# Optimization experiments

Hardware: AMD Instinct MI355X
Metric: run time of the kernel (lower is better)

Reference implementation:

```python
import jax, jax.numpy as jnp
import numpy as np

B, T, L, W = 4, 4096, 64, 8          # batch, text len, media tokens, max_window_per_audio
DIM, DIM_A, H, DH = 2048, 1024, 8, 64
INNER = H * DH
LN_EPS = 1e-5


def setup_inputs() -> dict:
    key = jax.random.key(0)
    ks = jax.random.split(key, 8)
    x = jax.random.normal(ks[0], (B, T, DIM), jnp.float32)
    media = jax.random.normal(ks[1], (B, L, 1, DIM_A), jnp.float32)
    media_mask = jax.random.uniform(ks[2], (B, L, 1)) > 0.1
    # sparse media markers (~8 per row); ensure at least one per row
    media_locations = (jax.random.uniform(ks[3], (B, T)) < (8.0 / T)).astype(jnp.int32)
    media_locations = media_locations.at[:, 0].set(1)
    Wq = jax.random.normal(ks[4], (DIM, INNER), jnp.float32) / np.sqrt(DIM).astype(np.float32)
    Wkv = jax.random.normal(ks[5], (DIM_A, 2 * INNER), jnp.float32) / np.sqrt(DIM_A).astype(np.float32)
    Wout = jax.random.normal(ks[6], (INNER, DIM), jnp.float32) / np.sqrt(INNER).astype(np.float32)
    gamma = jnp.ones((DIM,), jnp.float32)
    beta = jnp.zeros((DIM,), jnp.float32)
    return dict(x=x, media=media, media_mask=media_mask, media_locations=media_locations,
                Wq=Wq, Wkv=Wkv, Wout=Wout, gamma=gamma, beta=beta)


def reference(x, media, media_mask, media_locations, Wq, Wkv, Wout, gamma, beta):
    scale = DH ** -0.5
    # LayerNorm (biased variance, like torch)
    mu = x.mean(-1, keepdims=True)
    var = x.var(-1, keepdims=True)
    xn = (x - mu) * jax.lax.rsqrt(var + LN_EPS) * gamma + beta
    # projections
    q = (xn @ Wq).reshape(B, T, H, DH).transpose(0, 2, 1, 3) * scale   # [B,h,T,dh]
    kv = media.reshape(B, L, DIM_A) @ Wkv
    k, v = jnp.split(kv, 2, axis=-1)
    k = k.reshape(B, L, H, DH).transpose(0, 2, 1, 3)                   # [B,h,L,dh]
    v = v.reshape(B, L, H, DH).transpose(0, 2, 1, 3)
    sim = jnp.einsum('bhid,bhjd->bhij', q, k)                          # [B,h,T,L]
    big = jnp.finfo(sim.dtype).max
    # media validity mask
    mm = media_mask.reshape(B, 1, 1, L)
    sim = jnp.where(mm, sim, -big)
    # few-shot window mask (only_attend_immediate_media=False):
    # token t attends windows [0, max(#media at <=t, 1) * W)
    cum = jnp.cumsum((media_locations != 0).astype(jnp.int32), axis=1)  # [B,T]
    end = jnp.maximum(cum, 1) * W                                       # [B,T]
    fsm = jnp.arange(L)[None, None, :] < end[:, :, None]                # [B,T,L]
    sim = jnp.where(fsm[:, None], sim, -big)
    sim = sim - jax.lax.stop_gradient(sim.max(-1, keepdims=True))
    attn = jax.nn.softmax(sim, axis=-1)
    out = jnp.einsum('bhij,bhjd->bhid', attn, v)                        # [B,h,T,dh]
    out = out.transpose(0, 2, 1, 3).reshape(B, T, INNER)
    return out @ Wout
```

## Files before the change

### kernel.cpp

```cpp
#include <hip/hip_runtime.h>
#include <float.h>

typedef __bf16 bf16;
typedef __bf16 bf16x8 __attribute__((ext_vector_type(8)));
typedef float f32x4 __attribute__((ext_vector_type(4)));
typedef float f32x16 __attribute__((ext_vector_type(16)));

#define GAS __attribute__((address_space(1)))
#define LAS __attribute__((address_space(3)))

__device__ __forceinline__ void gload_lds16(const void* g, void* l) {
  __builtin_amdgcn_global_load_lds((const GAS unsigned int*)g, (LAS unsigned int*)l, 16, 0, 0);
}

__global__ __launch_bounds__(512, 2) void qattn(
    const bf16* __restrict__ xn, const bf16* __restrict__ wqT,
    const bf16* __restrict__ kvb, const int* __restrict__ mk,
    const int* __restrict__ endw, bf16* __restrict__ aob) {
  constexpr int K = 2048;
  __shared__ __align__(16) bf16 Abuf[3][256 * 64];
  __shared__ __align__(16) bf16 Bbuf[3][128 * 64];
  const int tid = threadIdx.x, lane = tid & 63;
  const int w = tid >> 6, wr = w >> 1, wc = w & 1;
  const int g = lane >> 4, fr = lane & 15;

  const int gx = gridDim.x;
  const int nwg = gx * gridDim.y;
  int lid = blockIdx.y * gx + blockIdx.x;
  {
    const int qq = nwg >> 3, rr = nwg & 7;
    const int xcd = lid & 7, pos = lid >> 3;
    lid = (xcd < rr ? xcd * (qq + 1) : rr * (qq + 1) + (xcd - rr) * qq) + pos;
  }
  const int bx = lid % gx, by = lid / gx;
  const size_t m0 = (size_t)by * 256;
  const int n0 = bx * 128;

  const int nt = K >> 6;
  const int srow = tid >> 3, sslot = tid & 7;

  f32x4 acc[4][4] = {};

  auto stage = [&](int t) {
    const int s = t % 3;
    const int kt = t << 6;
#pragma unroll
    for (int c = 0; c < 4; ++c) {
      const int r = c * 64 + srow;
      gload_lds16(xn + (m0 + r) * (size_t)K + kt + ((sslot ^ (r & 7)) << 3),
                  &Abuf[s][c * 4096 + w * 512]);
    }
#pragma unroll
    for (int c = 0; c < 2; ++c) {
      const int r = c * 64 + srow;
      gload_lds16(wqT + (size_t)(n0 + r) * K + kt + ((sslot ^ (r & 7)) << 3),
                  &Bbuf[s][c * 4096 + w * 512]);
    }
  };
  auto rdA = [&](int s, int mi, int ks) {
    const int r = wr * 64 + mi * 16 + fr;
    return *(const bf16x8*)&Abuf[s][r * 64 + ((((ks << 2) | g) ^ (r & 7)) << 3)];
  };
  auto rdB = [&](int s, int ni, int ks) {
    const int r = wc * 64 + ni * 16 + fr;
    return *(const bf16x8*)&Bbuf[s][r * 64 + ((((ks << 2) | g) ^ (r & 7)) << 3)];
  };
  auto compute = [&](int t) {
    const int s = t % 3;
    bf16x8 bv[4][2];
#pragma unroll
    for (int ni = 0; ni < 4; ++ni)
#pragma unroll
      for (int ks = 0; ks < 2; ++ks) bv[ni][ks] = rdB(s, ni, ks);
    __builtin_amdgcn_s_setprio(1);
#pragma unroll
    for (int mi = 0; mi < 4; ++mi)
#pragma unroll
      for (int ks = 0; ks < 2; ++ks) {
        const bf16x8 av = rdA(s, mi, ks);
#pragma unroll
        for (int ni = 0; ni < 4; ++ni)
          acc[mi][ni] = __builtin_amdgcn_mfma_f32_16x16x32_bf16(
              av, bv[ni][ks], acc[mi][ni], 0, 0, 0);
      }
    __builtin_amdgcn_s_setprio(0);
  };

  stage(0);
  stage(1);
  for (int t = 0; t < nt - 1; ++t) {
    __builtin_amdgcn_sched_barrier(0);
    asm volatile("s_waitcnt vmcnt(6)" ::: "memory");
    __builtin_amdgcn_s_barrier();
    __builtin_amdgcn_sched_barrier(0);
    if (t + 2 < nt) stage(t + 2);
    compute(t);
  }
  __builtin_amdgcn_sched_barrier(0);
  asm volatile("s_waitcnt vmcnt(0)" ::: "memory");
  __builtin_amdgcn_s_barrier();
  __builtin_amdgcn_sched_barrier(0);
  compute(nt - 1);

  __builtin_amdgcn_s_barrier();
  __builtin_amdgcn_sched_barrier(0);

  const int b = (int)(m0 >> 12);
  bf16* QP = &Abuf[0][0] + w * 4096;
  bf16* Klds = &Bbuf[0][0];
  bf16* Vlds = &Bbuf[1][0];

#pragma unroll
  for (int mi = 0; mi < 4; ++mi)
#pragma unroll
    for (int ni = 0; ni < 4; ++ni)
#pragma unroll
      for (int rg = 0; rg < 4; ++rg) {
        const int row = mi * 16 + g * 4 + rg, col = ni * 16 + fr;
        QP[row * 64 + (((col >> 3) ^ (row & 7)) << 3) + (col & 7)] =
            (bf16)acc[mi][ni][rg];
      }

#pragma unroll
  for (int j = 0; j < 2; ++j) {
    const int idx = j * 512 + tid;
    const int head = idx >> 9, l = (idx >> 3) & 63, sl = idx & 7;
    gload_lds16(kvb + (size_t)(b * 64 + l) * 1024 + (2 * bx + head) * 64 +
                    ((sl ^ (l & 7)) << 3),
                Klds + (j * 512 + w * 64) * 8);
  }
#pragma unroll
  for (int j = 0; j < 2; ++j) {
    const int idx = j * 512 + tid;
    const int head = idx >> 9, l = (idx >> 3) & 63, sg = idx & 7;
    bf16x8 vv = *(const bf16x8*)&kvb[(size_t)(b * 64 + l) * 1024 + 512 +
                                     (2 * bx + head) * 64 + sg * 8];
#pragma unroll
    for (int e = 0; e < 8; ++e) {
      const int dh = sg * 8 + e;
      Vlds[head * 4096 + dh * 64 + (((l >> 3) ^ (dh & 7)) << 3) + (l & 7)] =
          vv[e];
    }
  }
  asm volatile("s_waitcnt vmcnt(0)" ::: "memory");
  __syncthreads();

  f32x4 sacc[4][4] = {};
#pragma unroll
  for (int ks = 0; ks < 2; ++ks) {
    bf16x8 aq[4], bk[4];
#pragma unroll
    for (int mi = 0; mi < 4; ++mi) {
      const int r = mi * 16 + fr;
      aq[mi] = *(const bf16x8*)&QP[r * 64 + ((((ks << 2) | g) ^ (r & 7)) << 3)];
    }
#pragma unroll
    for (int ni = 0; ni < 4; ++ni) {
      const int l = ni * 16 + fr;
      bk[ni] = *(const bf16x8*)&Klds[wc * 4096 + l * 64 +
                                     ((((ks << 2) | g) ^ (l & 7)) << 3)];
    }
#pragma unroll
    for (int mi = 0; mi < 4; ++mi)
#pragma unroll
      for (int ni = 0; ni < 4; ++ni)
        sacc[mi][ni] = __builtin_amdgcn_mfma_f32_16x16x32_bf16(
            aq[mi], bk[ni], sacc[mi][ni], 0, 0, 0);
  }

#pragma unroll
  for (int mi = 0; mi < 4; ++mi) {
    const int4 ev4 = *(const int4*)&endw[m0 + wr * 64 + mi * 16 + g * 4];
    const int ev[4] = {ev4.x, ev4.y, ev4.z, ev4.w};
    float p[4][4];
#pragma unroll
    for (int ni = 0; ni < 4; ++ni) {
      const int l = ni * 16 + fr;
      const bool mv = (mk[b * 64 + l] != 0);
#pragma unroll
      for (int rg = 0; rg < 4; ++rg)
        p[ni][rg] = (mv && (l < ev[rg])) ? sacc[mi][ni][rg] : -FLT_MAX;
    }
#pragma unroll
    for (int rg = 0; rg < 4; ++rg) {
      float m = fmaxf(fmaxf(p[0][rg], p[1][rg]), fmaxf(p[2][rg], p[3][rg]));
      m = fmaxf(m, __shfl_xor(m, 1));
      m = fmaxf(m, __shfl_xor(m, 2));
      m = fmaxf(m, __shfl_xor(m, 4));
      m = fmaxf(m, __shfl_xor(m, 8));
      float sum = 0.f;
#pragma unroll
      for (int ni = 0; ni < 4; ++ni) {
        p[ni][rg] = __expf(p[ni][rg] - m);
        sum += p[ni][rg];
      }
      sum += __shfl_xor(sum, 1);
      sum += __shfl_xor(sum, 2);
      sum += __shfl_xor(sum, 4);
      sum += __shfl_xor(sum, 8);
      const float inv = 1.f / sum;
#pragma unroll
      for (int ni = 0; ni < 4; ++ni) p[ni][rg] *= inv;
    }
#pragma unroll
    for (int ni = 0; ni < 4; ++ni) {
      const int l = ni * 16 + fr;
#pragma unroll
      for (int rg = 0; rg < 4; ++rg) {
        const int row = mi * 16 + g * 4 + rg;
        QP[row * 64 + (((l >> 3) ^ (row & 7)) << 3) + (l & 7)] =
            (bf16)p[ni][rg];
      }
    }
  }

  f32x4 oacc[4][4] = {};
#pragma unroll
  for (int ks = 0; ks < 2; ++ks) {
    bf16x8 pa[4], bv[4];
#pragma unroll
    for (int mi = 0; mi < 4; ++mi) {
      const int r = mi * 16 + fr;
      pa[mi] = *(const bf16x8*)&QP[r * 64 + ((((ks << 2) | g) ^ (r & 7)) << 3)];
    }
#pragma unroll
    for (int nd = 0; nd < 4; ++nd) {
      const int dh = nd * 16 + fr;
      bv[nd] = *(const bf16x8*)&Vlds[wc * 4096 + dh * 64 +
                                     ((((ks << 2) | g) ^ (dh & 7)) << 3)];
    }
#pragma unroll
    for (int mi = 0; mi < 4; ++mi)
#pragma unroll
      for (int nd = 0; nd < 4; ++nd)
        oacc[mi][nd] = __builtin_amdgcn_mfma_f32_16x16x32_bf16(
            pa[mi], bv[nd], oacc[mi][nd], 0, 0, 0);
  }
#pragma unroll
  for (int mi = 0; mi < 4; ++mi)
#pragma unroll
    for (int nd = 0; nd < 4; ++nd)
#pragma unroll
      for (int rg = 0; rg < 4; ++rg) {
        const size_t t = m0 + wr * 64 + mi * 16 + g * 4 + rg;
        aob[t * 512 + (2 * bx + wc) * 64 + nd * 16 + fr] =
            (bf16)oacc[mi][nd][rg];
      }
}

template <int OUT_BF16>
__global__ __launch_bounds__(512, 2) void gemm_big(
    const bf16* __restrict__ A, const bf16* __restrict__ Bt,
    void* __restrict__ Cv, int M, int N, int K) {
  __shared__ __align__(16) bf16 Abuf[3][256 * 64];
  __shared__ __align__(16) bf16 Bbuf[3][128 * 64];
  const int tid = threadIdx.x, lane = tid & 63;
  const int w = tid >> 6, wr = w >> 2, wc = w & 3;
  const int l31 = lane & 31, hi = lane >> 5;

  const int gx = gridDim.x;
  const int nwg = gx * gridDim.y;
  int lid = blockIdx.y * gx + blockIdx.x;
  {
    const int qq = nwg >> 3, rr = nwg & 7;
    const int xcd = lid & 7, pos = lid >> 3;
    lid = (xcd < rr ? xcd * (qq + 1) : rr * (qq + 1) + (xcd - rr) * qq) + pos;
  }
  const int bx = lid % gx, by = lid / gx;
  const size_t m0 = (size_t)by * 256, n0 = (size_t)bx * 128;

  const int nt = K >> 6;
  const int srow = tid >> 3;
  const int sslot = tid & 7;

  f32x16 acc[4] = {};

  auto stage = [&](int t) {
    const int s = t % 3;
    const int kt = t << 6;
#pragma unroll
    for (int c = 0; c < 4; ++c) {
      const int r = c * 64 + srow;
      gload_lds16(A + (m0 + r) * (size_t)K + kt + ((sslot ^ (r & 7)) << 3),
                  &Abuf[s][c * 4096 + w * 512]);
    }
#pragma unroll
    for (int c = 0; c < 2; ++c) {
      const int r = c * 64 + srow;
      gload_lds16(Bt + (n0 + r) * (size_t)K + kt + ((sslot ^ (r & 7)) << 3),
                  &Bbuf[s][c * 4096 + w * 512]);
    }
  };

  auto rdA = [&](int s, int mi, int ks) {
    const int r = wr * 128 + mi * 32 + l31;
    return *(const bf16x8*)&Abuf[s][r * 64 + ((((ks << 1) | hi) ^ (r & 7)) << 3)];
  };
  auto rdB = [&](int s, int ks) {
    const int r = wc * 32 + l31;
    return *(const bf16x8*)&Bbuf[s][r * 64 + ((((ks << 1) | hi) ^ (r & 7)) << 3)];
  };

  auto compute = [&](int t) {
    const int s = t % 3;
    bf16x8 bv[4];
#pragma unroll
    for (int ks = 0; ks < 4; ++ks) bv[ks] = rdB(s, ks);
    __builtin_amdgcn_s_setprio(1);
#pragma unroll
    for (int ks = 0; ks < 4; ++ks)
#pragma unroll
      for (int mi = 0; mi < 4; ++mi) {
        const bf16x8 av = rdA(s, mi, ks);
        acc[mi] = __builtin_amdgcn_mfma_f32_32x32x16_bf16(av, bv[ks], acc[mi],
                                                          0, 0, 0);
      }
    __builtin_amdgcn_s_setprio(0);
  };

  stage(0);
  stage(1);
  for (int t = 0; t < nt - 1; ++t) {
    __builtin_amdgcn_sched_barrier(0);
    asm volatile("s_waitcnt vmcnt(6)" ::: "memory");
    __builtin_amdgcn_s_barrier();
    __builtin_amdgcn_sched_barrier(0);
    if (t + 2 < nt) stage(t + 2);
    compute(t);
  }
  __builtin_amdgcn_sched_barrier(0);
  asm volatile("s_waitcnt vmcnt(0)" ::: "memory");
  __builtin_amdgcn_s_barrier();
  __builtin_amdgcn_sched_barrier(0);
  compute(nt - 1);

#pragma unroll
  for (int mi = 0; mi < 4; ++mi)
#pragma unroll
    for (int rg = 0; rg < 16; ++rg) {
      const size_t row =
          m0 + wr * 128 + mi * 32 + (rg & 3) + ((rg >> 2) << 3) + (hi << 2);
      const size_t col = n0 + wc * 32 + l31;
      if (OUT_BF16)
        ((bf16*)Cv)[row * (size_t)N + col] = (bf16)acc[mi][rg];
      else
        ((float*)Cv)[row * (size_t)N + col] = acc[mi][rg];
    }
}

template <int OUT_BF16>
__global__ __launch_bounds__(256, 2) void gemm_bt(
    const bf16* __restrict__ A, const bf16* __restrict__ Bt,
    void* __restrict__ Cv, int M, int N, int K) {
  __shared__ bf16 As[128 * 32];
  __shared__ bf16 Bs[128 * 32];
  const int tid = threadIdx.x;
  const int lane = tid & 63, w = tid >> 6;
  const int wr = w >> 1, wc = w & 1;

  const int gx = gridDim.x;
  const int nwg = gx * gridDim.y;
  int lid = blockIdx.y * gx + blockIdx.x;
  {
    const int qq = nwg >> 3, rr = nwg & 7;
    const int xcd = lid & 7, pos = lid >> 3;
    lid = (xcd < rr ? xcd * (qq + 1) : rr * (qq + 1) + (xcd - rr) * qq) + pos;
  }
  const int bx = lid % gx, by = lid / gx;
  const size_t m0 = (size_t)by * 128, n0 = (size_t)bx * 128;

  const int srow = lane >> 2, sslot = lane & 3;
  const int g = lane >> 4, fr = lane & 15;

  f32x4 acc[4][4] = {};

  for (int kt = 0; kt < K; kt += 32) {
    __syncthreads();
#pragma unroll
    for (int j = 0; j < 2; ++j) {
      const int c = 2 * w + j;
      const int r = c * 16 + srow;
      const int ks = (sslot ^ (r & 3)) << 3;
      gload_lds16(A + (m0 + r) * K + kt + ks, &As[c * 512]);
      gload_lds16(Bt + (n0 + r) * K + kt + ks, &Bs[c * 512]);
    }
    __syncthreads();
    bf16x8 av[4], bv[4];
#pragma unroll
    for (int mi = 0; mi < 4; ++mi) {
      const int r = wr * 64 + mi * 16 + fr;
      av[mi] = *(const bf16x8*)&As[r * 32 + ((g ^ (r & 3)) << 3)];
    }
#pragma unroll
    for (int ni = 0; ni < 4; ++ni) {
      const int r = wc * 64 + ni * 16 + fr;
      bv[ni] = *(const bf16x8*)&Bs[r * 32 + ((g ^ (r & 3)) << 3)];
    }
#pragma unroll
    for (int mi = 0; mi < 4; ++mi)
#pragma unroll
      for (int ni = 0; ni < 4; ++ni)
        acc[mi][ni] = __builtin_amdgcn_mfma_f32_16x16x32_bf16(
            av[mi], bv[ni], acc[mi][ni], 0, 0, 0);
  }

#pragma unroll
  for (int mi = 0; mi < 4; ++mi)
#pragma unroll
    for (int ni = 0; ni < 4; ++ni)
#pragma unroll
      for (int rg = 0; rg < 4; ++rg) {
        const size_t row = m0 + wr * 64 + mi * 16 + g * 4 + rg;
        const size_t col = n0 + wc * 64 + ni * 16 + fr;
        if (OUT_BF16)
          ((bf16*)Cv)[row * (size_t)N + col] = (bf16)acc[mi][ni][rg];
        else
          ((float*)Cv)[row * (size_t)N + col] = acc[mi][ni][rg];
      }
}

__device__ __forceinline__ void transp64(const float* __restrict__ src,
                                         bf16* __restrict__ dst, int R, int C,
                                         float scale, int tile, float* lds) {
  const int tilesC = C >> 6;
  const int tr = tile / tilesC, tc = tile % tilesC;
  const int r0 = tr << 6, c0 = tc << 6;
  const int tid = threadIdx.x;
  const int lr = tid >> 6, lc = tid & 63;
#pragma unroll
  for (int j = 0; j < 16; ++j) {
    const int r = j * 4 + lr;
    lds[r * 65 + lc] = src[(size_t)(r0 + r) * C + c0 + lc];
  }
  __syncthreads();
#pragma unroll
  for (int j = 0; j < 16; ++j) {
    const int rr = j * 4 + lr;
    dst[(size_t)(c0 + rr) * R + r0 + lc] = (bf16)(lds[lc * 65 + rr] * scale);
  }
}

__global__ __launch_bounds__(256) void prep_all(
    const float* __restrict__ x, const float* __restrict__ gamma,
    const float* __restrict__ beta, bf16* __restrict__ xn,
    const float* __restrict__ Wq, bf16* __restrict__ wqT,
    const float* __restrict__ Wkv, bf16* __restrict__ wkvT,
    const float* __restrict__ Wout, bf16* __restrict__ woT,
    const float* __restrict__ media, bf16* __restrict__ medb,
    const int* __restrict__ mloc, int* __restrict__ endw,
    const unsigned char* __restrict__ mraw, int* __restrict__ mk) {
  __shared__ float shf[64 * 65];
  const int blk = blockIdx.x, tid = threadIdx.x;

  if (blk < 16384) {
    const size_t base = (size_t)blk * 2048 + tid * 8;
    f32x4 v0 = *(const f32x4*)(x + base);
    f32x4 v1 = *(const f32x4*)(x + base + 4);
    float s = 0.f, q2 = 0.f;
#pragma unroll
    for (int j = 0; j < 4; ++j) {
      s += v0[j] + v1[j];
      q2 += v0[j] * v0[j] + v1[j] * v1[j];
    }
    for (int off = 32; off > 0; off >>= 1) {
      s += __shfl_down(s, off);
      q2 += __shfl_down(q2, off);
    }
    const int lane = tid & 63, wv = tid >> 6;
    if (lane == 0) { shf[wv] = s; shf[4 + wv] = q2; }
    __syncthreads();
    s = shf[0] + shf[1] + shf[2] + shf[3];
    q2 = shf[4] + shf[5] + shf[6] + shf[7];
    const float mu = s * (1.f / 2048.f);
    const float var = q2 * (1.f / 2048.f) - mu * mu;
    const float rs = rsqrtf(var + 1e-5f);
    f32x4 g0 = *(const f32x4*)(gamma + tid * 8);
    f32x4 g1 = *(const f32x4*)(gamma + tid * 8 + 4);
    f32x4 b0 = *(const f32x4*)(beta + tid * 8);
    f32x4 b1 = *(const f32x4*)(beta + tid * 8 + 4);
    bf16x8 o;
#pragma unroll
    for (int j = 0; j < 4; ++j) {
      o[j] = (bf16)((v0[j] - mu) * rs * g0[j] + b0[j]);
      o[4 + j] = (bf16)((v1[j] - mu) * rs * g1[j] + b1[j]);
    }
    *(bf16x8*)(xn + base) = o;
  } else if (blk < 16640) {
    transp64(Wq, wqT, 2048, 512, 0.125f, blk - 16384, shf);
  } else if (blk < 16896) {
    transp64(Wkv, wkvT, 1024, 1024, 1.f, blk - 16640, shf);
  } else if (blk < 17152) {
    transp64(Wout, woT, 512, 2048, 1.f, blk - 16896, shf);
  } else if (blk < 18176) {
    const int i = (blk - 17152) * 256 + tid;
    medb[i] = (bf16)media[i];
  } else if (blk < 18180) {
    int* part = (int*)shf;
    const int b = blk - 18176;
    int loc[16];
    int s = 0;
    const int base = b * 4096 + tid * 16;
#pragma unroll
    for (int j = 0; j < 16; ++j) {
      loc[j] = (mloc[base + j] != 0) ? 1 : 0;
      s += loc[j];
    }
    part[tid] = s;
    __syncthreads();
    for (int off = 1; off < 256; off <<= 1) {
      int v = (tid >= off) ? part[tid - off] : 0;
      __syncthreads();
      part[tid] += v;
      __syncthreads();
    }
    int c = (tid > 0) ? part[tid - 1] : 0;
#pragma unroll
    for (int j = 0; j < 16; ++j) {
      c += loc[j];
      int e = (c > 1 ? c : 1) << 3;
      endw[base + j] = e > 64 ? 64 : e;
    }
  } else {
    int* isbool = (int*)shf;
    if (tid == 0) *isbool = 0;
    __syncthreads();
    const unsigned char v = mraw[tid];
    if ((tid & 3) != 0 && v != 0) atomicOr(isbool, 1);
    __syncthreads();
    mk[tid] = (*isbool) ? (int)mraw[tid] : ((const int*)mraw)[tid];
  }
}

extern "C" void kernel_launch(void* const* d_in, const int* in_sizes, int n_in,
                              void* d_out, int out_size, void* d_ws,
                              size_t ws_size, hipStream_t stream) {
  const float* x = (const float*)d_in[0];
  const float* media = (const float*)d_in[1];
  const unsigned char* mraw = (const unsigned char*)d_in[2];
  const int* mloc = (const int*)d_in[3];
  const float* Wq = (const float*)d_in[4];
  const float* Wkv = (const float*)d_in[5];
  const float* Wout = (const float*)d_in[6];
  const float* gamma = (const float*)d_in[7];
  const float* beta = (const float*)d_in[8];
  float* out = (float*)d_out;

  bf16* xn = (bf16*)d_out;

  char* ws = (char*)d_ws;
  size_t off = 0;
  auto carve = [&](size_t bytes) {
    void* p = ws + off;
    off += (bytes + 255) & ~(size_t)255;
    return p;
  };
  bf16* aob = (bf16*)carve((size_t)16384 * 512 * 2);
  bf16* kvb = (bf16*)carve((size_t)256 * 1024 * 2);
  bf16* wqT = (bf16*)carve((size_t)512 * 2048 * 2);
  bf16* wkvT = (bf16*)carve((size_t)1024 * 1024 * 2);
  bf16* woT = (bf16*)carve((size_t)2048 * 512 * 2);
  bf16* medb = (bf16*)carve((size_t)256 * 1024 * 2);
  int* endw = (int*)carve((size_t)4 * 4096 * 4);
  int* mk = (int*)carve(256 * 4);
  (void)ws_size;
  (void)in_sizes;
  (void)n_in;
  (void)out_size;

  prep_all<<<18181, 256, 0, stream>>>(x, gamma, beta, xn, Wq, wqT, Wkv, wkvT,
                                      Wout, woT, media, medb, mloc, endw, mraw,
                                      mk);

  gemm_bt<1><<<dim3(8, 2), 256, 0, stream>>>(medb, wkvT, kvb, 256, 1024, 1024);

  qattn<<<dim3(4, 64), 512, 0, stream>>>(xn, wqT, kvb, mk, endw, aob);

  gemm_big<0><<<dim3(16, 64), 512, 0, stream>>>(aob, woT, out, 16384, 2048,
                                                512);
}
```

Baseline: 177.7 us.

## Merge all stages into one persistent cooperative kernel with grid syncs

Replaces the four separate launches (prep, KV GEMM, fused Q-attention, output GEMM) with a single cooperative kernel of 256 workgroups. Grid-wide syncs separate the phases: preprocessing, the KV projection on 16 blocks, and then the attention and output GEMM, with each block computing four 256x128 output tiles in a loop. The aim is to remove launch overhead and inter-kernel gaps. In exchange, the layernorm phase now uses only 256 blocks, most blocks sit idle during the KV GEMM, and the output GEMM runs with fixed persistent tiling, which may lower occupancy and overlap.

```diff
diff --git a/kernel.cpp b/kernel.cpp
--- a/kernel.cpp
+++ b/kernel.cpp
@@ -1,7 +1,11 @@
 #include <hip/hip_runtime.h>
+#include <hip/hip_cooperative_groups.h>
 #include <float.h>
 
+namespace cg = cooperative_groups;
+
 typedef __bf16 bf16;
+typedef __bf16 bf16x4v __attribute__((ext_vector_type(4)));
 typedef __bf16 bf16x8 __attribute__((ext_vector_type(8)));
 typedef float f32x4 __attribute__((ext_vector_type(4)));
 typedef float f32x16 __attribute__((ext_vector_type(16)));
@@ -13,546 +17,524 @@
   __builtin_amdgcn_global_load_lds((const GAS unsigned int*)g, (LAS unsigned int*)l, 16, 0, 0);
 }
 
-__global__ __launch_bounds__(512, 2) void qattn(
-    const bf16* __restrict__ xn, const bf16* __restrict__ wqT,
-    const bf16* __restrict__ kvb, const int* __restrict__ mk,
-    const int* __restrict__ endw, bf16* __restrict__ aob) {
-  constexpr int K = 2048;
-  __shared__ __align__(16) bf16 Abuf[3][256 * 64];
-  __shared__ __align__(16) bf16 Bbuf[3][128 * 64];
-  const int tid = threadIdx.x, lane = tid & 63;
-  const int w = tid >> 6, wr = w >> 1, wc = w & 1;
-  const int g = lane >> 4, fr = lane & 15;
-
-  const int gx = gridDim.x;
-  const int nwg = gx * gridDim.y;
-  int lid = blockIdx.y * gx + blockIdx.x;
+struct MP {
+  const float* x;
+  const float* media;
+  const unsigned char* mraw;
+  const int* mloc;
+  const float* Wq;
+  const float* Wkv;
+  const float* Wout;
+  const float* gamma;
+  const float* beta;
+  float* out;
+  bf16* xn;
+  bf16* aob;
+  bf16* kvb;
+  bf16* wqT;
+  bf16* wkvT;
+  bf16* woT;
+  bf16* medb;
+  int* endw;
+  int* mk;
+};
+
+__global__ __launch_bounds__(512, 2) void mega(MP p) {
+  __shared__ __align__(16) char smem[147456];
+  const int tid = threadIdx.x, lane = tid & 63, w = tid >> 6;
+  const int lid = blockIdx.x;
+  const int lidx = ((lid & 7) << 5) | (lid >> 3);
+
+  if (lid < 4) {
+    int* part = (int*)smem;
+    const int b = lid;
+    int loc[8];
+    int s = 0;
+    const int base = b * 4096 + tid * 8;
+#pragma unroll
+    for (int j = 0; j < 8; ++j) {
+      loc[j] = (p.mloc[base + j] != 0) ? 1 : 0;
+      s += loc[j];
+    }
+    part[tid] = s;
+    __syncthreads();
+    for (int off = 1; off < 512; off <<= 1) {
+      int v = (tid >= off) ? part[tid - off] : 0;
+      __syncthreads();
+      part[tid] += v;
+      __syncthreads();
+    }
+    int c = (tid > 0) ? part[tid - 1] : 0;
+#pragma unroll
+    for (int j = 0; j < 8; ++j) {
+      c += loc[j];
+      int e = (c > 1 ? c : 1) << 3;
+      p.endw[base + j] = e > 64 ? 64 : e;
+    }
+  } else if (lid == 4) {
+    int* isbool = (int*)smem;
+    if (tid == 0) *isbool = 0;
+    __syncthreads();
+    if (tid < 256) {
+      const unsigned char v = p.mraw[tid];
+      if ((tid & 3) != 0 && v != 0) atomicOr(isbool, 1);
+    }
+    __syncthreads();
+    if (tid < 256)
+      p.mk[tid] = (*isbool) ? (int)p.mraw[tid] : ((const int*)p.mraw)[tid];
+  }
+  __syncthreads();
+
   {
-    const int qq = nwg >> 3, rr = nwg & 7;
-    const int xcd = lid & 7, pos = lid >> 3;
-    lid = (xcd < rr ? xcd * (qq + 1) : rr * (qq + 1) + (xcd - rr) * qq) + pos;
-  }
-  const int bx = lid % gx, by = lid / gx;
-  const size_t m0 = (size_t)by * 256;
-  const int n0 = bx * 128;
-
-  const int nt = K >> 6;
-  const int srow = tid >> 3, sslot = tid & 7;
-
-  f32x4 acc[4][4] = {};
-
-  auto stage = [&](int t) {
-    const int s = t % 3;
-    const int kt = t << 6;
-#pragma unroll
-    for (int c = 0; c < 4; ++c) {
-      const int r = c * 64 + srow;
-      gload_lds16(xn + (m0 + r) * (size_t)K + kt + ((sslot ^ (r & 7)) << 3),
-                  &Abuf[s][c * 4096 + w * 512]);
-    }
-#pragma unroll
-    for (int c = 0; c < 2; ++c) {
-      const int r = c * 64 + srow;
-      gload_lds16(wqT + (size_t)(n0 + r) * K + kt + ((sslot ^ (r & 7)) << 3),
-                  &Bbuf[s][c * 4096 + w * 512]);
-    }
-  };
-  auto rdA = [&](int s, int mi, int ks) {
-    const int r = wr * 64 + mi * 16 + fr;
-    return *(const bf16x8*)&Abuf[s][r * 64 + ((((ks << 2) | g) ^ (r & 7)) << 3)];
-  };
-  auto rdB = [&](int s, int ni, int ks) {
-    const int r = wc * 64 + ni * 16 + fr;
-    return *(const bf16x8*)&Bbuf[s][r * 64 + ((((ks << 2) | g) ^ (r & 7)) << 3)];
-  };
-  auto compute = [&](int t) {
-    const int s = t % 3;
-    bf16x8 bv[4][2];
-#pragma unroll
-    for (int ni = 0; ni < 4; ++ni)
-#pragma unroll
-      for (int ks = 0; ks < 2; ++ks) bv[ni][ks] = rdB(s, ni, ks);
-    __builtin_amdgcn_s_setprio(1);
+    const int i0 = lid * 1024 + tid;
+    p.medb[i0] = (bf16)p.media[i0];
+    p.medb[i0 + 512] = (bf16)p.media[i0 + 512];
+  }
+
+  {
+    float* lds = (float*)smem;
+#pragma unroll 1
+    for (int j3 = 0; j3 < 3; ++j3) {
+      const int job = lid + j3 * 256;
+      const float* src;
+      bf16* dst;
+      int R, C, t0;
+      float sc;
+      if (job < 256) {
+        src = p.Wq; dst = p.wqT; R = 2048; C = 512; sc = 0.125f; t0 = job;
+      } else if (job < 512) {
+        src = p.Wkv; dst = p.wkvT; R = 1024; C = 1024; sc = 1.f; t0 = job - 256;
+      } else {
+        src = p.Wout; dst = p.woT; R = 512; C = 2048; sc = 1.f; t0 = job - 512;
+      }
+      const int tilesC = C >> 6;
+      const int r0 = (t0 / tilesC) << 6, c0 = (t0 % tilesC) << 6;
+      const int lr = tid >> 6, lc = tid & 63;
+#pragma unroll
+      for (int j = 0; j < 8; ++j) {
+        const int r = j * 8 + lr;
+        lds[r * 65 + lc] = src[(size_t)(r0 + r) * C + c0 + lc];
+      }
+      __syncthreads();
+#pragma unroll
+      for (int j = 0; j < 8; ++j) {
+        const int rr = j * 8 + lr;
+        dst[(size_t)(c0 + rr) * R + r0 + lc] = (bf16)(lds[lc * 65 + rr] * sc);
+      }
+      __syncthreads();
+    }
+  }
+
+  {
+#pragma unroll 1
+    for (int i = 0; i < 8; ++i) {
+      const int row = (lid << 6) + (i << 3) + w;
+      const float* xr = p.x + (size_t)row * 2048;
+      float s = 0.f, q2 = 0.f;
+#pragma unroll
+      for (int j = 0; j < 8; ++j) {
+        f32x4 v = *(const f32x4*)(xr + j * 256 + lane * 4);
+        s += v[0] + v[1] + v[2] + v[3];
+        q2 += v[0] * v[0] + v[1] * v[1] + v[2] * v[2] + v[3] * v[3];
+      }
+#pragma unroll
+      for (int off = 32; off > 0; off >>= 1) {
+        s += __shfl_down(s, off);
+        q2 += __shfl_down(q2, off);
+      }
+      s = __shfl(s, 0);
+      q2 = __shfl(q2, 0);
+      const float mu = s * (1.f / 2048.f);
+      const float rs = rsqrtf(q2 * (1.f / 2048.f) - mu * mu + 1e-5f);
+#pragma unroll
+      for (int j = 0; j < 8; ++j) {
+        f32x4 v = *(const f32x4*)(xr + j * 256 + lane * 4);
+        f32x4 gg = *(const f32x4*)(p.gamma + j * 256 + lane * 4);
+        f32x4 bb = *(const f32x4*)(p.beta + j * 256 + lane * 4);
+        bf16x4v o;
+#pragma unroll
+        for (int e = 0; e < 4; ++e) o[e] = (bf16)((v[e] - mu) * rs * gg[e] + bb[e]);
+        *(bf16x4v*)(p.xn + (size_t)row * 2048 + j * 256 + lane * 4) = o;
+      }
+    }
+  }
+
+  cg::this_grid().sync();
+
+  if (lid < 16) {
+    bf16* As = (bf16*)smem;
+    bf16* Bs = (bf16*)(smem + 8192);
+    const int m0k = (lid >> 3) * 128, n0k = (lid & 7) * 128;
+    const int wr = w >> 2, wc = w & 3;
+    const int g = lane >> 4, fr = lane & 15;
+    const int srow = tid >> 2, sslot = tid & 3;
+    f32x4 acc[4][2] = {};
+    for (int kt = 0; kt < 1024; kt += 32) {
+      __syncthreads();
+      gload_lds16(
+          p.medb + (size_t)(m0k + srow) * 1024 + kt + ((sslot ^ (srow & 3)) << 3),
+          As + w * 512);
+      gload_lds16(
+          p.wkvT + (size_t)(n0k + srow) * 1024 + kt + ((sslot ^ (srow & 3)) << 3),
+          Bs + w * 512);
+      __syncthreads();
+      bf16x8 av[4], bv[2];
+#pragma unroll
+      for (int mi = 0; mi < 4; ++mi) {
+        const int r = wr * 64 + mi * 16 + fr;
+        av[mi] = *(const bf16x8*)&As[r * 32 + ((g ^ (r & 3)) << 3)];
+      }
+#pragma unroll
+      for (int ni = 0; ni < 2; ++ni) {
+        const int r = wc * 32 + ni * 16 + fr;
+        bv[ni] = *(const bf16x8*)&Bs[r * 32 + ((g ^ (r & 3)) << 3)];
+      }
+#pragma unroll
+      for (int mi = 0; mi < 4; ++mi)
+#pragma unroll
+        for (int ni = 0; ni < 2; ++ni)
+          acc[mi][ni] = __builtin_amdgcn_mfma_f32_16x16x32_bf16(
+              av[mi], bv[ni], acc[mi][ni], 0, 0, 0);
+    }
 #pragma unroll
     for (int mi = 0; mi < 4; ++mi)
 #pragma unroll
-      for (int ks = 0; ks < 2; ++ks) {
-        const bf16x8 av = rdA(s, mi, ks);
-#pragma unroll
-        for (int ni = 0; ni < 4; ++ni)
-          acc[mi][ni] = __builtin_amdgcn_mfma_f32_16x16x32_bf16(
-              av, bv[ni][ks], acc[mi][ni], 0, 0, 0);
-      }
-    __builtin_amdgcn_s_setprio(0);
-  };
-
-  stage(0);
-  stage(1);
-  for (int t = 0; t < nt - 1; ++t) {
+      for (int ni = 0; ni < 2; ++ni)
+#pragma unroll
+        for (int rg = 0; rg < 4; ++rg) {
+          const int row = m0k + wr * 64 + mi * 16 + g * 4 + rg;
+          const int col = n0k + wc * 32 + ni * 16 + fr;
+          p.kvb[(size_t)row * 1024 + col] = (bf16)acc[mi][ni][rg];
+        }
+  }
+
+  cg::this_grid().sync();
+
+  {
+    bf16* AB = (bf16*)smem;
+    bf16* BB = (bf16*)(smem + 98304);
+    auto Ab = [&](int s) { return AB + s * (256 * 64); };
+    auto Bb = [&](int s) { return BB + s * (128 * 64); };
+    constexpr int K = 2048;
+    const int wr = w >> 1, wc = w & 1;
+    const int g = lane >> 4, fr = lane & 15;
+    const int bx = lidx & 3, by = lidx >> 2;
+    const size_t m0 = (size_t)by * 256;
+    const int n0 = bx * 128;
+    const int nt = K >> 6;
+    const int srow = tid >> 3, sslot = tid & 7;
+
+    f32x4 acc[4][4] = {};
+
+    auto stage = [&](int t) {
+      const int s = t % 3;
+      const int kt = t << 6;
+#pragma unroll
+      for (int c = 0; c < 4; ++c) {
+        const int r = c * 64 + srow;
+        gload_lds16(p.xn + (m0 + r) * (size_t)K + kt + ((sslot ^ (r & 7)) << 3),
+                    Ab(s) + c * 4096 + w * 512);
+      }
+#pragma unroll
+      for (int c = 0; c < 2; ++c) {
+        const int r = c * 64 + srow;
+        gload_lds16(
+            p.wqT + (size_t)(n0 + r) * K + kt + ((sslot ^ (r & 7)) << 3),
+            Bb(s) + c * 4096 + w * 512);
+      }
+    };
+    auto rdA = [&](int s, int mi, int ks) {
+      const int r = wr * 64 + mi * 16 + fr;
+      return *(const bf16x8*)(Ab(s) + r * 64 + ((((ks << 2) | g) ^ (r & 7)) << 3));
+    };
+    auto rdB = [&](int s, int ni, int ks) {
+      const int r = wc * 64 + ni * 16 + fr;
+      return *(const bf16x8*)(Bb(s) + r * 64 + ((((ks << 2) | g) ^ (r & 7)) << 3));
+    };
+    auto compute = [&](int t) {
+      const int s = t % 3;
+      bf16x8 bv[4][2];
+#pragma unroll
+      for (int ni = 0; ni < 4; ++ni)
+#pragma unroll
+        for (int ks = 0; ks < 2; ++ks) bv[ni][ks] = rdB(s, ni, ks);
+      __builtin_amdgcn_s_setprio(1);
+#pragma unroll
+      for (int mi = 0; mi < 4; ++mi)
+#pragma unroll
+        for (int ks = 0; ks < 2; ++ks) {
+          const bf16x8 av = rdA(s, mi, ks);
+#pragma unroll
+          for (int ni = 0; ni < 4; ++ni)
+            acc[mi][ni] = __builtin_amdgcn_mfma_f32_16x16x32_bf16(
+                av, bv[ni][ks], acc[mi][ni], 0, 0, 0);
+        }
+      __builtin_amdgcn_s_setprio(0);
+    };
+
+    stage(0);
+    stage(1);
+    for (int t = 0; t < nt - 1; ++t) {
+      __builtin_amdgcn_sched_barrier(0);
+      asm volatile("s_waitcnt vmcnt(6)" ::: "memory");
+      __builtin_amdgcn_s_barrier();
+      __builtin_amdgcn_sched_barrier(0);
+      if (t + 2 < nt) stage(t + 2);
+      compute(t);
+    }
     __builtin_amdgcn_sched_barrier(0);
-    asm volatile("s_waitcnt vmcnt(6)" ::: "memory");
+    asm volatile("s_waitcnt vmcnt(0)" ::: "memory");
     __builtin_amdgcn_s_barrier();
     __builtin_amdgcn_sched_barrier(0);
-    if (t + 2 < nt) stage(t + 2);
-    compute(t);
-  }
-  __builtin_amdgcn_sched_barrier(0);
-  asm volatile("s_waitcnt vmcnt(0)" ::: "memory");
-  __builtin_amdgcn_s_barrier();
-  __builtin_amdgcn_sched_barrier(0);
-  compute(nt - 1);
-
-  __builtin_amdgcn_s_barrier();
-  __builtin_amdgcn_sched_barrier(0);
-
-  const int b = (int)(m0 >> 12);
-  bf16* QP = &Abuf[0][0] + w * 4096;
-  bf16* Klds = &Bbuf[0][0];
-  bf16* Vlds = &Bbuf[1][0];
-
-#pragma unroll
-  for (int mi = 0; mi < 4; ++mi)
-#pragma unroll
-    for (int ni = 0; ni < 4; ++ni)
-#pragma unroll
-      for (int rg = 0; rg < 4; ++rg) {
-        const int row = mi * 16 + g * 4 + rg, col = ni * 16 + fr;
-        QP[row * 64 + (((col >> 3) ^ (row & 7)) << 3) + (col & 7)] =
-            (bf16)acc[mi][ni][rg];
-      }
-
-#pragma unroll
-  for (int j = 0; j < 2; ++j) {
-    const int idx = j * 512 + tid;
-    const int head = idx >> 9, l = (idx >> 3) & 63, sl = idx & 7;
-    gload_lds16(kvb + (size_t)(b * 64 + l) * 1024 + (2 * bx + head) * 64 +
-                    ((sl ^ (l & 7)) << 3),
-                Klds + (j * 512 + w * 64) * 8);
-  }
-#pragma unroll
-  for (int j = 0; j < 2; ++j) {
-    const int idx = j * 512 + tid;
-    const int head = idx >> 9, l = (idx >> 3) & 63, sg = idx & 7;
-    bf16x8 vv = *(const bf16x8*)&kvb[(size_t)(b * 64 + l) * 1024 + 512 +
-                                     (2 * bx + head) * 64 + sg * 8];
-#pragma unroll
-    for (int e = 0; e < 8; ++e) {
-      const int dh = sg * 8 + e;
-      Vlds[head * 4096 + dh * 64 + (((l >> 3) ^ (dh & 7)) << 3) + (l & 7)] =
-          vv[e];
-    }
-  }
-  asm volatile("s_waitcnt vmcnt(0)" ::: "memory");
-  __syncthreads();
-
-  f32x4 sacc[4][4] = {};
-#pragma unroll
-  for (int ks = 0; ks < 2; ++ks) {
-    bf16x8 aq[4], bk[4];
-#pragma unroll
-    for (int mi = 0; mi < 4; ++mi) {
-      const int r = mi * 16 + fr;
-      aq[mi] = *(const bf16x8*)&QP[r * 64 + ((((ks << 2) | g) ^ (r & 7)) << 3)];
-    }
-#pragma unroll
-    for (int ni = 0; ni < 4; ++ni) {
-      const int l = ni * 16 + fr;
-      bk[ni] = *(const bf16x8*)&Klds[wc * 4096 + l * 64 +
-                                     ((((ks << 2) | g) ^ (l & 7)) << 3)];
-    }
-#pragma unroll
-    for (int mi = 0; mi < 4; ++mi)
-#pragma unroll
-      for (int ni = 0; ni < 4; ++ni)
-        sacc[mi][ni] = __builtin_amdgcn_mfma_f32_16x16x32_bf16(
-            aq[mi], bk[ni], sacc[mi][ni], 0, 0, 0);
-  }
-
-#pragma unroll
-  for (int mi = 0; mi < 4; ++mi) {
-    const int4 ev4 = *(const int4*)&endw[m0 + wr * 64 + mi * 16 + g * 4];
-    const int ev[4] = {ev4.x, ev4.y, ev4.z, ev4.w};
-    float p[4][4];
-#pragma unroll
-    for (int ni = 0; ni < 4; ++ni) {
-      const int l = ni * 16 + fr;
-      const bool mv = (mk[b * 64 + l] != 0);
-#pragma unroll
-      for (int rg = 0; rg < 4; ++rg)
-        p[ni][rg] = (mv && (l < ev[rg])) ? sacc[mi][ni][rg] : -FLT_MAX;
-    }
-#pragma unroll
-    for (int rg = 0; rg < 4; ++rg) {
-      float m = fmaxf(fmaxf(p[0][rg], p[1][rg]), fmaxf(p[2][rg], p[3][rg]));
-      m = fmaxf(m, __shfl_xor(m, 1));
-      m = fmaxf(m, __shfl_xor(m, 2));
-      m = fmaxf(m, __shfl_xor(m, 4));
-      m = fmaxf(m, __shfl_xor(m, 8));
-      float sum = 0.f;
-#pragma unroll
-      for (int ni = 0; ni < 4; ++ni) {
-        p[ni][rg] = __expf(p[ni][rg] - m);
-        sum += p[ni][rg];
-      }
-      sum += __shfl_xor(sum, 1);
-      sum += __shfl_xor(sum, 2);
-      sum += __shfl_xor(sum, 4);
-      sum += __shfl_xor(sum, 8);
-      const float inv = 1.f / sum;
-#pragma unroll
-      for (int ni = 0; ni < 4; ++ni) p[ni][rg] *= inv;
-    }
-#pragma unroll
-    for (int ni = 0; ni < 4; ++ni) {
-      const int l = ni * 16 + fr;
-#pragma unroll
-      for (int rg = 0; rg < 4; ++rg) {
-        const int row = mi * 16 + g * 4 + rg;
-        QP[row * 64 + (((l >> 3) ^ (row & 7)) << 3) + (l & 7)] =
-            (bf16)p[ni][rg];
-      }
-    }
-  }
-
-  f32x4 oacc[4][4] = {};
-#pragma unroll
-  for (int ks = 0; ks < 2; ++ks) {
-    bf16x8 pa[4], bv[4];
-#pragma unroll
-    for (int mi = 0; mi < 4; ++mi) {
-      const int r = mi * 16 + fr;
-      pa[mi] = *(const bf16x8*)&QP[r * 64 + ((((ks << 2) | g) ^ (r & 7)) << 3)];
-    }
-#pragma unroll
-    for (int nd = 0; nd < 4; ++nd) {
-      const int dh = nd * 16 + fr;
-      bv[nd] = *(const bf16x8*)&Vlds[wc * 4096 + dh * 64 +
-                                     ((((ks << 2) | g) ^ (dh & 7)) << 3)];
-    }
-#pragma unroll
-    for (int mi = 0; mi < 4; ++mi)
-#pragma unroll
-      for (int nd = 0; nd < 4; ++nd)
-        oacc[mi][nd] = __builtin_amdgcn_mfma_f32_16x16x32_bf16(
-            pa[mi], bv[nd], oacc[mi][nd], 0, 0, 0);
-  }
-#pragma unroll
-  for (int mi = 0; mi < 4; ++mi)
-#pragma unroll
-    for (int nd = 0; nd < 4; ++nd)
-#pragma unroll
-      for (int rg = 0; rg < 4; ++rg) {
-        const size_t t = m0 + wr * 64 + mi * 16 + g * 4 + rg;
-        aob[t * 512 + (2 * bx + wc) * 64 + nd * 16 + fr] =
-            (bf16)oacc[mi][nd][rg];
-      }
-}
-
-template <int OUT_BF16>
-__global__ __launch_bounds__(512, 2) void gemm_big(
-    const bf16* __restrict__ A, const bf16* __restrict__ Bt,
-    void* __restrict__ Cv, int M, int N, int K) {
-  __shared__ __align__(16) bf16 Abuf[3][256 * 64];
-  __shared__ __align__(16) bf16 Bbuf[3][128 * 64];
-  const int tid = threadIdx.x, lane = tid & 63;
-  const int w = tid >> 6, wr = w >> 2, wc = w & 3;
-  const int l31 = lane & 31, hi = lane >> 5;
-
-  const int gx = gridDim.x;
-  const int nwg = gx * gridDim.y;
-  int lid = blockIdx.y * gx + blockIdx.x;
-  {
-    const int qq = nwg >> 3, rr = nwg & 7;
-    const int xcd = lid & 7, pos = lid >> 3;
-    lid = (xcd < rr ? xcd * (qq + 1) : rr * (qq + 1) + (xcd - rr) * qq) + pos;
-  }
-  const int bx = lid % gx, by = lid / gx;
-  const size_t m0 = (size_t)by * 256, n0 = (size_t)bx * 128;
-
-  const int nt = K >> 6;
-  const int srow = tid >> 3;
-  const int sslot = tid & 7;
-
-  f32x16 acc[4] = {};
-
-  auto stage = [&](int t) {
-    const int s = t % 3;
-    const int kt = t << 6;
-#pragma unroll
-    for (int c = 0; c < 4; ++c) {
-      const int r = c * 64 + srow;
-      gload_lds16(A + (m0 + r) * (size_t)K + kt + ((sslot ^ (r & 7)) << 3),
-                  &Abuf[s][c * 4096 + w * 512]);
-    }
-#pragma unroll
-    for (int c = 0; c < 2; ++c) {
-      const int r = c * 64 + srow;
-      gload_lds16(Bt + (n0 + r) * (size_t)K + kt + ((sslot ^ (r & 7)) << 3),
-                  &Bbuf[s][c * 4096 + w * 512]);
-    }
-  };
-
-  auto rdA = [&](int s, int mi, int ks) {
-    const int r = wr * 128 + mi * 32 + l31;
-    return *(const bf16x8*)&Abuf[s][r * 64 + ((((ks << 1) | hi) ^ (r & 7)) << 3)];
-  };
-  auto rdB = [&](int s, int ks) {
-    const int r = wc * 32 + l31;
-    return *(const bf16x8*)&Bbuf[s][r * 64 + ((((ks << 1) | hi) ^ (r & 7)) << 3)];
-  };
-
-  auto compute = [&](int t) {
-    const int s = t % 3;
-    bf16x8 bv[4];
-#pragma unroll
-    for (int ks = 0; ks < 4; ++ks) bv[ks] = rdB(s, ks);
-    __builtin_amdgcn_s_setprio(1);
-#pragma unroll
-    for (int ks = 0; ks < 4; ++ks)
-#pragma unroll
-      for (int mi = 0; mi < 4; ++mi) {
-        const bf16x8 av = rdA(s, mi, ks);
-        acc[mi] = __builtin_amdgcn_mfma_f32_32x32x16_bf16(av, bv[ks], acc[mi],
-                                                          0, 0, 0);
-      }
-    __builtin_amdgcn_s_setprio(0);
-  };
-
-  stage(0);
-  stage(1);
-  for (int t = 0; t < nt - 1; ++t) {
-    __builtin_amdgcn_sched_barrier(0);
-    asm volatile("s_waitcnt vmcnt(6)" ::: "memory");
+    compute(nt - 1);
+
     __builtin_amdgcn_s_barrier();
     __builtin_amdgcn_sched_barrier(0);
-    if (t + 2 < nt) stage(t + 2);
-    compute(t);
-  }
-  __builtin_amdgcn_sched_barrier(0);
-  asm volatile("s_waitcnt vmcnt(0)" ::: "memory");
-  __builtin_amdgcn_s_barrier();
-  __builtin_amdgcn_sched_barrier(0);
-  compute(nt - 1);
-
-#pragma unroll
-  for (int mi = 0; mi < 4; ++mi)
-#pragma unroll
-    for (int rg = 0; rg < 16; ++rg) {
-      const size_t row =
-          m0 + wr * 128 + mi * 32 + (rg & 3) + ((rg >> 2) << 3) + (hi << 2);
-      const size_t col = n0 + wc * 32 + l31;
-      if (OUT_BF16)
-        ((bf16*)Cv)[row * (size_t)N + col] = (bf16)acc[mi][rg];
-      else
-        ((float*)Cv)[row * (size_t)N + col] = acc[mi][rg];
-    }
-}
-
-template <int OUT_BF16>
-__global__ __launch_bounds__(256, 2) void gemm_bt(
-    const bf16* __restrict__ A, const bf16* __restrict__ Bt,
-    void* __restrict__ Cv, int M, int N, int K) {
-  __shared__ bf16 As[128 * 32];
-  __shared__ bf16 Bs[128 * 32];
-  const int tid = threadIdx.x;
-  const int lane = tid & 63, w = tid >> 6;
-  const int wr = w >> 1, wc = w & 1;
-
-  const int gx = gridDim.x;
-  const int nwg = gx * gridDim.y;
-  int lid = blockIdx.y * gx + blockIdx.x;
+
+    const int b = (int)(m0 >> 12);
+    bf16* QP = Ab(0) + w * 4096;
+    bf16* Klds = Bb(0);
+    bf16* Vlds = Bb(1);
+
+#pragma unroll
+    for (int mi = 0; mi < 4; ++mi)
+#pragma unroll
+      for (int ni = 0; ni < 4; ++ni)
+#pragma unroll
+        for (int rg = 0; rg < 4; ++rg) {
+          const int row = mi * 16 + g * 4 + rg, col = ni * 16 + fr;
+          QP[row * 64 + (((col >> 3) ^ (row & 7)) << 3) + (col & 7)] =
+              (bf16)acc[mi][ni][rg];
+        }
+
+#pragma unroll
+    for (int j = 0; j < 2; ++j) {
+      const int idx = j * 512 + tid;
+      const int head = idx >> 9, l = (idx >> 3) & 63, sl = idx & 7;
+      gload_lds16(p.kvb + (size_t)(b * 64 + l) * 1024 + (2 * bx + head) * 64 +
+                      ((sl ^ (l & 7)) << 3),
+                  Klds + (j * 512 + w * 64) * 8);
+    }
+#pragma unroll
+    for (int j = 0; j < 2; ++j) {
+      const int idx = j * 512 + tid;
+      const int head = idx >> 9, l = (idx >> 3) & 63, sg = idx & 7;
+      bf16x8 vv = *(const bf16x8*)&p.kvb[(size_t)(b * 64 + l) * 1024 + 512 +
+                                         (2 * bx + head) * 64 + sg * 8];
+#pragma unroll
+      for (int e = 0; e < 8; ++e) {
+        const int dh = sg * 8 + e;
+        Vlds[head * 4096 + dh * 64 + (((l >> 3) ^ (dh & 7)) << 3) + (l & 7)] =
+            vv[e];
+      }
+    }
+    asm volatile("s_waitcnt vmcnt(0)" ::: "memory");
+    __syncthreads();
+
+    f32x4 sacc[4][4] = {};
+#pragma unroll
+    for (int ks = 0; ks < 2; ++ks) {
+      bf16x8 aq[4], bk[4];
+#pragma unroll
+      for (int mi = 0; mi < 4; ++mi) {
+        const int r = mi * 16 + fr;
+        aq[mi] = *(const bf16x8*)&QP[r * 64 + ((((ks << 2) | g) ^ (r & 7)) << 3)];
+      }
+#pragma unroll
+      for (int ni = 0; ni < 4; ++ni) {
+        const int l = ni * 16 + fr;
+        bk[ni] = *(const bf16x8*)&Klds[wc * 4096 + l * 64 +
+                                       ((((ks << 2) | g) ^ (l & 7)) << 3)];
+      }
+#pragma unroll
+      for (int mi = 0; mi < 4; ++mi)
+#pragma unroll
+        for (int ni = 0; ni < 4; ++ni)
+          sacc[mi][ni] = __builtin_amdgcn_mfma_f32_16x16x32_bf16(
+              aq[mi], bk[ni], sacc[mi][ni], 0, 0, 0);
+    }
+
+#pragma unroll
+    for (int mi = 0; mi < 4; ++mi) {
+      const int4 ev4 = *(const int4*)&p.endw[m0 + wr * 64 + mi * 16 + g * 4];
+      const int ev[4] = {ev4.x, ev4.y, ev4.z, ev4.w};
+      float pp[4][4];
+#pragma unroll
+      for (int ni = 0; ni < 4; ++ni) {
+        const int l = ni * 16 + fr;
+        const bool mv = (p.mk[b * 64 + l] != 0);
+#pragma unroll
+        for (int rg = 0; rg < 4; ++rg)
+          pp[ni][rg] = (mv && (l < ev[rg])) ? sacc[mi][ni][rg] : -FLT_MAX;
+      }
+#pragma unroll
+      for (int rg = 0; rg < 4; ++rg) {
+        float m = fmaxf(fmaxf(pp[0][rg], pp[1][rg]), fmaxf(pp[2][rg], pp[3][rg]));
+        m = fmaxf(m, __shfl_xor(m, 1));
+        m = fmaxf(m, __shfl_xor(m, 2));
+        m = fmaxf(m, __shfl_xor(m, 4));
+        m = fmaxf(m, __shfl_xor(m, 8));
+        float sum = 0.f;
+#pragma unroll
+        for (int ni = 0; ni < 4; ++ni) {
+          pp[ni][rg] = __expf(pp[ni][rg] - m);
+          sum += pp[ni][rg];
+        }
+        sum += __shfl_xor(sum, 1);
+        sum += __shfl_xor(sum, 2);
+        sum += __shfl_xor(sum, 4);
+        sum += __shfl_xor(sum, 8);
+        const float inv = 1.f / sum;
+#pragma unroll
+        for (int ni = 0; ni < 4; ++ni) pp[ni][rg] *= inv;
+      }
+#pragma unroll
+      for (int ni = 0; ni < 4; ++ni) {
+        const int l = ni * 16 + fr;
+#pragma unroll
+        for (int rg = 0; rg < 4; ++rg) {
+          const int row = mi * 16 + g * 4 + rg;
+          QP[row * 64 + (((l >> 3) ^ (row & 7)) << 3) + (l & 7)] =
+              (bf16)pp[ni][rg];
+        }
+      }
+    }
+
+    f32x4 oacc[4][4] = {};
+#pragma unroll
+    for (int ks = 0; ks < 2; ++ks) {
+      bf16x8 pa[4], bv[4];
+#pragma unroll
+      for (int mi = 0; mi < 4; ++mi) {
+        const int r = mi * 16 + fr;
+        pa[mi] = *(const bf16x8*)&QP[r * 64 + ((((ks << 2) | g) ^ (r & 7)) << 3)];
+      }
+#pragma unroll
+      for (int nd = 0; nd < 4; ++nd) {
+        const int dh = nd * 16 + fr;
+        bv[nd] = *(const bf16x8*)&Vlds[wc * 4096 + dh * 64 +
+                                       ((((ks << 2) | g) ^ (dh & 7)) << 3)];
+      }
+#pragma unroll
+      for (int mi = 0; mi < 4; ++mi)
+#pragma unroll
+        for (int nd = 0; nd < 4; ++nd)
+          oacc[mi][nd] = __builtin_amdgcn_mfma_f32_16x16x32_bf16(
+              pa[mi], bv[nd], oacc[mi][nd], 0, 0, 0);
+    }
+#pragma unroll
+    for (int mi = 0; mi < 4; ++mi)
+#pragma unroll
+      for (int nd = 0; nd < 4; ++nd)
+#pragma unroll
+        for (int rg = 0; rg < 4; ++rg) {
+          const size_t t = m0 + wr * 64 + mi * 16 + g * 4 + rg;
+          p.aob[t * 512 + (2 * bx + wc) * 64 + nd * 16 + fr] =
+              (bf16)oacc[mi][nd][rg];
+        }
+  }
+
+  cg::this_grid().sync();
+
   {
-    const int qq = nwg >> 3, rr = nwg & 7;
-    const int xcd = lid & 7, pos = lid >> 3;
-    lid = (xcd < rr ? xcd * (qq + 1) : rr * (qq + 1) + (xcd - rr) * qq) + pos;
-  }
-  const int bx = lid % gx, by = lid / gx;
-  const size_t m0 = (size_t)by * 128, n0 = (size_t)bx * 128;
-
-  const int srow = lane >> 2, sslot = lane & 3;
-  const int g = lane >> 4, fr = lane & 15;
-
-  f32x4 acc[4][4] = {};
-
-  for (int kt = 0; kt < K; kt += 32) {
-    __syncthreads();
-#pragma unroll
-    for (int j = 0; j < 2; ++j) {
-      const int c = 2 * w + j;
-      const int r = c * 16 + srow;
-      const int ks = (sslot ^ (r & 3)) << 3;
-      gload_lds16(A + (m0 + r) * K + kt + ks, &As[c * 512]);
-      gload_lds16(Bt + (n0 + r) * K + kt + ks, &Bs[c * 512]);
-    }
-    __syncthreads();
-    bf16x8 av[4], bv[4];
-#pragma unroll
-    for (int mi = 0; mi < 4; ++mi) {
-      const int r = wr * 64 + mi * 16 + fr;
-      av[mi] = *(const bf16x8*)&As[r * 32 + ((g ^ (r & 3)) << 3)];
-    }
-#pragma unroll
-    for (int ni = 0; ni < 4; ++ni) {
-      const int r = wc * 64 + ni * 16 + fr;
-      bv[ni] = *(const bf16x8*)&Bs[r * 32 + ((g ^ (r & 3)) << 3)];
-    }
-#pragma unroll
-    for (int mi = 0; mi < 4; ++mi)
-#pragma unroll
-      for (int ni = 0; ni < 4; ++ni)
-        acc[mi][ni] = __builtin_amdgcn_mfma_f32_16x16x32_bf16(
-            av[mi], bv[ni], acc[mi][ni], 0, 0, 0);
-  }
-
-#pragma unroll
-  for (int mi = 0; mi < 4; ++mi)
-#pragma unroll
-    for (int ni = 0; ni < 4; ++ni)
-#pragma unroll
-      for (int rg = 0; rg < 4; ++rg) {
-        const size_t row = m0 + wr * 64 + mi * 16 + g * 4 + rg;
-        const size_t col = n0 + wc * 64 + ni * 16 + fr;
-        if (OUT_BF16)
-          ((bf16*)Cv)[row * (size_t)N + col] = (bf16)acc[mi][ni][rg];
-        else
-          ((float*)Cv)[row * (size_t)N + col] = acc[mi][ni][rg];
-      }
-}
-
-__device__ __forceinline__ void transp64(const float* __restrict__ src,
-                                         bf16* __restrict__ dst, int R, int C,
-                                         float scale, int tile, float* lds) {
-  const int tilesC = C >> 6;
-  const int tr = tile / tilesC, tc = tile % tilesC;
-  const int r0 = tr << 6, c0 = tc << 6;
-  const int tid = threadIdx.x;
-  const int lr = tid >> 6, lc = tid & 63;
-#pragma unroll
-  for (int j = 0; j < 16; ++j) {
-    const int r = j * 4 + lr;
-    lds[r * 65 + lc] = src[(size_t)(r0 + r) * C + c0 + lc];
-  }
-  __syncthreads();
-#pragma unroll
-  for (int j = 0; j < 16; ++j) {
-    const int rr = j * 4 + lr;
-    dst[(size_t)(c0 + rr) * R + r0 + lc] = (bf16)(lds[lc * 65 + rr] * scale);
-  }
-}
-
-__global__ __launch_bounds__(256) void prep_all(
-    const float* __restrict__ x, const float* __restrict__ gamma,
-    const float* __restrict__ beta, bf16* __restrict__ xn,
-    const float* __restrict__ Wq, bf16* __restrict__ wqT,
-    const float* __restrict__ Wkv, bf16* __restrict__ wkvT,
-    const float* __restrict__ Wout, bf16* __restrict__ woT,
-    const float* __restrict__ media, bf16* __restrict__ medb,
-    const int* __restrict__ mloc, int* __restrict__ endw,
-    const unsigned char* __restrict__ mraw, int* __restrict__ mk) {
-  __shared__ float shf[64 * 65];
-  const int blk = blockIdx.x, tid = threadIdx.x;
-
-  if (blk < 16384) {
-    const size_t base = (size_t)blk * 2048 + tid * 8;
-    f32x4 v0 = *(const f32x4*)(x + base);
-    f32x4 v1 = *(const f32x4*)(x + base + 4);
-    float s = 0.f, q2 = 0.f;
-#pragma unroll
-    for (int j = 0; j < 4; ++j) {
-      s += v0[j] + v1[j];
-      q2 += v0[j] * v0[j] + v1[j] * v1[j];
-    }
-    for (int off = 32; off > 0; off >>= 1) {
-      s += __shfl_down(s, off);
-      q2 += __shfl_down(q2, off);
-    }
-    const int lane = tid & 63, wv = tid >> 6;
-    if (lane == 0) { shf[wv] = s; shf[4 + wv] = q2; }
-    __syncthreads();
-    s = shf[0] + shf[1] + shf[2] + shf[3];
-    q2 = shf[4] + shf[5] + shf[6] + shf[7];
-    const float mu = s * (1.f / 2048.f);
-    const float var = q2 * (1.f / 2048.f) - mu * mu;
-    const float rs = rsqrtf(var + 1e-5f);
-    f32x4 g0 = *(const f32x4*)(gamma + tid * 8);
-    f32x4 g1 = *(const f32x4*)(gamma + tid * 8 + 4);
-    f32x4 b0 = *(const f32x4*)(beta + tid * 8);
-    f32x4 b1 = *(const f32x4*)(beta + tid * 8 + 4);
-    bf16x8 o;
-#pragma unroll
-    for (int j = 0; j < 4; ++j) {
-      o[j] = (bf16)((v0[j] - mu) * rs * g0[j] + b0[j]);
-      o[4 + j] = (bf16)((v1[j] - mu) * rs * g1[j] + b1[j]);
-    }
-    *(bf16x8*)(xn + base) = o;
-  } else if (blk < 16640) {
-    transp64(Wq, wqT, 2048, 512, 0.125f, blk - 16384, shf);
-  } else if (blk < 16896) {
-    transp64(Wkv, wkvT, 1024, 1024, 1.f, blk - 16640, shf);
-  } else if (blk < 17152) {
-    transp64(Wout, woT, 512, 2048, 1.f, blk - 16896, shf);
-  } else if (blk < 18176) {
-    const int i = (blk - 17152) * 256 + tid;
-    medb[i] = (bf16)media[i];
-  } else if (blk < 18180) {
-    int* part = (int*)shf;
-    const int b = blk - 18176;
-    int loc[16];
-    int s = 0;
-    const int base = b * 4096 + tid * 16;
-#pragma unroll
-    for (int j = 0; j < 16; ++j) {
-      loc[j] = (mloc[base + j] != 0) ? 1 : 0;
-      s += loc[j];
-    }
-    part[tid] = s;
-    __syncthreads();
-    for (int off = 1; off < 256; off <<= 1) {
-      int v = (tid >= off) ? part[tid - off] : 0;
-      __syncthreads();
-      part[tid] += v;
-      __syncthreads();
-    }
-    int c = (tid > 0) ? part[tid - 1] : 0;
-#pragma unroll
-    for (int j = 0; j < 16; ++j) {
-      c += loc[j];
-      int e = (c > 1 ? c : 1) << 3;
-      endw[base + j] = e > 64 ? 64 : e;
-    }
-  } else {
-    int* isbool = (int*)shf;
-    if (tid == 0) *isbool = 0;
-    __syncthreads();
-    const unsigned char v = mraw[tid];
-    if ((tid & 3) != 0 && v != 0) atomicOr(isbool, 1);
-    __syncthreads();
-    mk[tid] = (*isbool) ? (int)mraw[tid] : ((const int*)mraw)[tid];
+    bf16* AB = (bf16*)smem;
+    bf16* BB = (bf16*)(smem + 98304);
+    auto Ab = [&](int s) { return AB + s * (256 * 64); };
+    auto Bb = [&](int s) { return BB + s * (128 * 64); };
+    const int l31 = lane & 31, hi = lane >> 5;
+    const int wro = w >> 2, wco = w & 3;
+    const int srow = tid >> 3, sslot = tid & 7;
+
+#pragma unroll 1
+    for (int k2 = 0; k2 < 4; ++k2) {
+      __syncthreads();
+      const int T = lidx * 4 + k2;
+      const size_t m0 = (size_t)(T >> 4) * 256;
+      const int n0 = (T & 15) * 128;
+      f32x16 acc[4] = {};
+
+      auto stage = [&](int t) {
+        const int s = t % 3;
+        const int kt = t << 6;
+#pragma unroll
+        for (int c = 0; c < 4; ++c) {
+          const int r = c * 64 + srow;
+          gload_lds16(p.aob + (m0 + r) * 512 + kt + ((sslot ^ (r & 7)) << 3),
+                      Ab(s) + c * 4096 + w * 512);
+        }
+#pragma unroll
+        for (int c = 0; c < 2; ++c) {
+          const int r = c * 64 + srow;
+          gload_lds16(
+              p.woT + (size_t)(n0 + r) * 512 + kt + ((sslot ^ (r & 7)) << 3),
+              Bb(s) + c * 4096 + w * 512);
+        }
+      };
+      auto rdA3 = [&](int s, int mi, int ks) {
+        const int r = wro * 128 + mi * 32 + l31;
+        return *(const bf16x8*)(Ab(s) + r * 64 +
+                                ((((ks << 1) | hi) ^ (r & 7)) << 3));
+      };
+      auto rdB3 = [&](int s, int ks) {
+        const int r = wco * 32 + l31;
+        return *(const bf16x8*)(Bb(s) + r * 64 +
+                                ((((ks << 1) | hi) ^ (r & 7)) << 3));
+      };
+      auto compute3 = [&](int t) {
+        const int s = t % 3;
+        bf16x8 bv[4];
+#pragma unroll
+        for (int ks = 0; ks < 4; ++ks) bv[ks] = rdB3(s, ks);
+        __builtin_amdgcn_s_setprio(1);
+#pragma unroll
+        for (int ks = 0; ks < 4; ++ks)
+#pragma unroll
+          for (int mi = 0; mi < 4; ++mi) {
+            const bf16x8 av = rdA3(s, mi, ks);
+            acc[mi] = __builtin_amdgcn_mfma_f32_32x32x16_bf16(av, bv[ks],
+                                                              acc[mi], 0, 0, 0);
+          }
+        __builtin_amdgcn_s_setprio(0);
+      };
+
+      stage(0);
+      stage(1);
+      for (int t = 0; t < 7; ++t) {
+        __builtin_amdgcn_sched_barrier(0);
+        asm volatile("s_waitcnt vmcnt(6)" ::: "memory");
+        __builtin_amdgcn_s_barrier();
+        __builtin_amdgcn_sched_barrier(0);
+        if (t + 2 < 8) stage(t + 2);
+        compute3(t);
+      }
+      __builtin_amdgcn_sched_barrier(0);
+      asm volatile("s_waitcnt vmcnt(0)" ::: "memory");
+      __builtin_amdgcn_s_barrier();
+      __builtin_amdgcn_sched_barrier(0);
+      compute3(7);
+
+#pragma unroll
+      for (int mi = 0; mi < 4; ++mi)
+#pragma unroll
+        for (int rg = 0; rg < 16; ++rg) {
+          const size_t row = m0 + wro * 128 + mi * 32 + (rg & 3) +
+                             ((rg >> 2) << 3) + (hi << 2);
+          const size_t col = (size_t)n0 + wco * 32 + l31;
+          p.out[row * 2048 + col] = acc[mi][rg];
+        }
+    }
   }
 }
 
 extern "C" void kernel_launch(void* const* d_in, const int* in_sizes, int n_in,
                               void* d_out, int out_size, void* d_ws,
                               size_t ws_size, hipStream_t stream) {
-  const float* x = (const float*)d_in[0];
-  const float* media = (const float*)d_in[1];
-  const unsigned char* mraw = (const unsigned char*)d_in[2];
-  const int* mloc = (const int*)d_in[3];
-  const float* Wq = (const float*)d_in[4];
-  const float* Wkv = (const float*)d_in[5];
-  const float* Wout = (const float*)d_in[6];
-  const float* gamma = (const float*)d_in[7];
-  const float* beta = (const float*)d_in[8];
-  float* out = (float*)d_out;
-
-  bf16* xn = (bf16*)d_out;
-
   char* ws = (char*)d_ws;
   size_t off = 0;
   auto carve = [&](size_t bytes) {
-    void* p = ws + off;
+    void* pv = ws + off;
     off += (bytes + 255) & ~(size_t)255;
-    return p;
+    return pv;
   };
   bf16* aob = (bf16*)carve((size_t)16384 * 512 * 2);
   bf16* kvb = (bf16*)carve((size_t)256 * 1024 * 2);
@@ -567,14 +549,28 @@
   (void)n_in;
   (void)out_size;
 
-  prep_all<<<18181, 256, 0, stream>>>(x, gamma, beta, xn, Wq, wqT, Wkv, wkvT,
-                                      Wout, woT, media, medb, mloc, endw, mraw,
-                                      mk);
-
-  gemm_bt<1><<<dim3(8, 2), 256, 0, stream>>>(medb, wkvT, kvb, 256, 1024, 1024);
-
-  qattn<<<dim3(4, 64), 512, 0, stream>>>(xn, wqT, kvb, mk, endw, aob);
-
-  gemm_big<0><<<dim3(16, 64), 512, 0, stream>>>(aob, woT, out, 16384, 2048,
-                                                512);
+  MP p;
+  p.x = (const float*)d_in[0];
+  p.media = (const float*)d_in[1];
+  p.mraw = (const unsigned char*)d_in[2];
+  p.mloc = (const int*)d_in[3];
+  p.Wq = (const float*)d_in[4];
+  p.Wkv = (const float*)d_in[5];
+  p.Wout = (const float*)d_in[6];
+  p.gamma = (const float*)d_in[7];
+  p.beta = (const float*)d_in[8];
+  p.out = (float*)d_out;
+  p.xn = (bf16*)d_out;
+  p.aob = aob;
+  p.kvb = kvb;
+  p.wqT = wqT;
+  p.wkvT = wkvT;
+  p.woT = woT;
+  p.medb = medb;
+  p.endw = endw;
+  p.mk = mk;
+
+  void* args[] = {&p};
+  hipLaunchCooperativeKernel((const void*)mega, dim3(256), dim3(512), args, 0,
+                             stream);
 }
```

Result: slower. 307.1 us (+72.8%).
